# Optimization experiments

Hardware: AMD Instinct MI355X
Metric: run time of the kernel (lower is better)

The kernel has to match this reference:

```python
import jax, jax.numpy as jnp
import numpy as np

VOCAB, SEQ, D_IN, HID, N_CLS, BATCH = 50257, 128, 768, 512, 9, 256


def setup_inputs() -> dict:
    key = jax.random.key(0)
    ks = jax.random.split(key, 12)
    s = 0.02
    return {
        "input_ids": jax.random.randint(ks[0], (BATCH, SEQ), 0, VOCAB),
        "tok_emb": jax.random.normal(ks[1], (VOCAB, D_IN), jnp.float32) * s,
        "pos_emb": jax.random.normal(ks[2], (SEQ, D_IN), jnp.float32) * s,
        # stacked per-gate Linear weights, gate order (i, f, g, o); Linear stores (out, in)
        "W1": jax.random.normal(ks[3], (4, HID, D_IN), jnp.float32) * s,
        "R1": jax.random.normal(ks[4], (4, HID, HID), jnp.float32) * s,
        "b1": jax.random.normal(ks[5], (4, HID), jnp.float32) * s,
        "W2": jax.random.normal(ks[6], (4, HID, HID), jnp.float32) * s,
        "R2": jax.random.normal(ks[7], (4, HID, HID), jnp.float32) * s,
        "b2": jax.random.normal(ks[8], (4, HID), jnp.float32) * s,
        "Wo": jax.random.normal(ks[9], (N_CLS, HID), jnp.float32) * s,
        "bo": jax.random.normal(ks[10], (N_CLS,), jnp.float32) * s,
    }


def _cell(x, h, c, W, R, b):
    # all four gate linears fused into one einsum each for x and h
    g = jnp.einsum('bi,ghi->gbh', x, W) + jnp.einsum('bj,ghj->gbh', h, R) + b[:, None, :]
    i = jax.nn.sigmoid(g[0])
    f = jax.nn.sigmoid(g[1])
    m = jnp.tanh(g[2])
    o = jax.nn.sigmoid(g[3])
    c_next = m * i + f * c
    h_next = o * jnp.tanh(c_next)
    return h_next, c_next


def reference(input_ids, tok_emb, pos_emb, W1, R1, b1, W2, R2, b2, Wo, bo):
    embeds = tok_emb[input_ids] + pos_emb[None, :, :]  # (B, S, D)
    B = embeds.shape[0]
    H = R1.shape[-1]
    x_seq = jnp.swapaxes(embeds, 0, 1)  # (S, B, D)
    init = tuple(jnp.zeros((B, H), embeds.dtype) for _ in range(4))

    def step(carry, x_t):
        h1, c1, h2, c2 = carry
        h1, c1 = _cell(x_t, h1, c1, W1, R1, b1)
        h2, c2 = _cell(h1, h2, c2, W2, R2, b2)
        out = h2 @ Wo.T + bo  # (B, num_class)
        return (h1, c1, h2, c2), out

    _, outs = jax.lax.scan(step, init, x_seq)  # (S, B, C)
    return jnp.swapaxes(outs, 0, 1)  # (B, S, C)
```

## Files before the change

### kernel.cpp

```cpp
#include <hip/hip_runtime.h>
#include <hip/hip_bf16.h>
#include <stdint.h>

#define BATCH_ 256
#define SEQ_   128
#define DIN_   768
#define HID_   512
#define NG_    2048
#define NCLS_  9

typedef unsigned short u16;
typedef unsigned int u32;
typedef unsigned long long u64;
typedef __attribute__((ext_vector_type(8))) short bf16x8;
typedef __attribute__((ext_vector_type(4))) float f32x4;

__device__ __forceinline__ float bf2f(u16 u) {
  return __builtin_bit_cast(float, (uint32_t)u << 16);
}
__device__ __forceinline__ u16 f2bf(float f) {
  uint32_t x = __builtin_bit_cast(uint32_t, f);
  uint32_t r = (x + 0x7fffu + ((x >> 16) & 1u)) >> 16;
  return (u16)r;
}

__device__ __forceinline__ void gload_lds16(const void* g, void* l) {
#if defined(__has_builtin)
#if __has_builtin(__builtin_amdgcn_global_load_lds)
  __builtin_amdgcn_global_load_lds((const __attribute__((address_space(1))) void*)g,
                                   (__attribute__((address_space(3))) void*)l, 16, 0, 0);
  return;
#endif
#endif
  *(uint4*)l = *(const uint4*)g;
}

__device__ __forceinline__ u32 aload32(const u32* p) {
  return __hip_atomic_load(p, __ATOMIC_RELAXED, __HIP_MEMORY_SCOPE_AGENT);
}
__device__ __forceinline__ void astore32(u32* p, u32 v) {
  __hip_atomic_store(p, v, __ATOMIC_RELAXED, __HIP_MEMORY_SCOPE_AGENT);
}

__global__ void castk(const float* __restrict__ s, u16* __restrict__ d, int n4) {
  int i = blockIdx.x * blockDim.x + threadIdx.x;
  if (i < n4) {
    float4 v = ((const float4*)s)[i];
    ushort4 o;
    o.x = f2bf(v.x); o.y = f2bf(v.y); o.z = f2bf(v.z); o.w = f2bf(v.w);
    ((ushort4*)d)[i] = o;
  }
}

__global__ __launch_bounds__(192) void embed_k(const int* __restrict__ ids,
                                               const float* __restrict__ tok,
                                               const float* __restrict__ pos,
                                               u16* __restrict__ X) {
  const int row = blockIdx.x;
  const int t = row >> 8, b = row & 255;
  const int id = ids[b * SEQ_ + t];
  const float4* tr = (const float4*)(tok + (size_t)id * DIN_);
  const float4* pr = (const float4*)(pos + (size_t)t * DIN_);
  const int i = threadIdx.x;
  float4 v = tr[i], p = pr[i];
  ushort4 o;
  o.x = f2bf(v.x + p.x); o.y = f2bf(v.y + p.y);
  o.z = f2bf(v.z + p.z); o.w = f2bf(v.w + p.w);
  ((ushort4*)(X + (size_t)row * DIN_))[i] = o;
}

__global__ __launch_bounds__(256) void gemm_bt(const u16* __restrict__ A,
                                               const u16* __restrict__ Bm,
                                               const float* __restrict__ bias,
                                               u16* __restrict__ C,
                                               int M, int N, int K) {
  __shared__ __align__(16) u16 As[128 * 64];
  __shared__ __align__(16) u16 Bs[128 * 64];
  const int tid = threadIdx.x;
  const int lane = tid & 63;
  const int wave = tid >> 6;
  const int m0 = blockIdx.y * 128;
  const int n0 = blockIdx.x * 128;
  const int wm = (wave >> 1) * 64;
  const int wn = (wave & 1) * 64;
  const int lr = lane & 15;
  const int lg = lane >> 4;
  f32x4 acc[4][4] = {};

  for (int k0 = 0; k0 < K; k0 += 64) {
#pragma unroll
    for (int it = 0; it < 4; ++it) {
      int e = it * 256 + tid;
      int r = e >> 3, c8 = (e & 7) * 8;
      gload_lds16(A + (size_t)(m0 + r) * K + k0 + c8, &As[e * 8]);
      gload_lds16(Bm + (size_t)(n0 + r) * K + k0 + c8, &Bs[e * 8]);
    }
    __syncthreads();
#pragma unroll
    for (int kk = 0; kk < 64; kk += 32) {
      bf16x8 af[4], bfr[4];
#pragma unroll
      for (int i = 0; i < 4; ++i) {
        af[i]  = *(const bf16x8*)&As[(wm + i * 16 + lr) * 64 + kk + lg * 8];
        bfr[i] = *(const bf16x8*)&Bs[(wn + i * 16 + lr) * 64 + kk + lg * 8];
      }
#pragma unroll
      for (int i = 0; i < 4; ++i)
#pragma unroll
        for (int j = 0; j < 4; ++j)
          acc[i][j] = __builtin_amdgcn_mfma_f32_16x16x32_bf16(af[i], bfr[j], acc[i][j], 0, 0, 0);
    }
    __syncthreads();
  }
#pragma unroll
  for (int i = 0; i < 4; ++i) {
#pragma unroll
    for (int j = 0; j < 4; ++j) {
      int col = n0 + wn + j * 16 + lr;
      float bv = bias[col];
#pragma unroll
      for (int q = 0; q < 4; ++q) {
        int row = m0 + wm + i * 16 + lg * 4 + q;
        C[(size_t)row * N + col] = f2bf(acc[i][j][q] + bv);
      }
    }
  }
}

__device__ __forceinline__ void stage64(char* dst, const u16* src, int tid) {
  const u64* s64 = (const u64*)src;
#pragma unroll
  for (int i = 0; i < 16; ++i) {
    int e = i * 512 + tid, r = e >> 7, c8 = e & 127;
    u64 v = s64[(size_t)r * 128 + c8];
    *(u64*)(dst + r * 1024 + ((((c8 >> 1) ^ (r & 7)) << 4) | ((c8 & 1) << 3))) = v;
  }
}

__global__ __launch_bounds__(512, 2) void lstm_duo2(
    const u16* __restrict__ Xpre,
    u16* __restrict__ H1,
    u16* __restrict__ H2,
    const u16* __restrict__ R1b,
    const u16* __restrict__ W2b,
    const u16* __restrict__ R2b,
    const float* __restrict__ b2,
    u32* __restrict__ flag1, u32* __restrict__ flag2) {
  __shared__ __align__(16) char lds[131072];
  const int tid = threadIdx.x;
  const int lane = tid & 63;
  const int w = tid >> 6;
  const int lr = lane & 15, lg = lane >> 4;
  const int kind = blockIdx.x >> 7;
  const int lb = blockIdx.x & 127;
  const int m4 = lb & 3, j32 = lb >> 2;
  const int m0 = m4 * 64, j0 = j32 * 16;
  const int g = w & 3, kh = w >> 2;
  const int cr = tid >> 3, cc = (tid & 7) * 2;
  float* Gsf = (float*)lds;
  char* As1 = lds;
  char* As2 = lds + 65536;

#define GS(KH, GG, RR, CC) Gsf[(((KH) * 4 + (GG)) * 64 + (RR)) * 17 + (CC)]

  if (kind == 0) {
    bf16x8 B1[8];
#pragma unroll
    for (int k = 0; k < 8; ++k)
      B1[k] = *(const bf16x8*)&R1b[(size_t)(g * 512 + j0 + lr) * 512 +
                                   kh * 256 + k * 32 + lg * 8];
    float cst0 = 0.f, cst1 = 0.f;

    for (int t = 0; t < SEQ_; ++t) {
      u32 xp[4];
#pragma unroll
      for (int gg = 0; gg < 4; ++gg)
        xp[gg] = *(const u32*)(Xpre + (size_t)t * (BATCH_ * NG_) +
                               (size_t)(m0 + cr) * NG_ + gg * 512 + j0 + cc);
      if (t > 0) {
        if (w == 0) {
          const u32* f = flag1 + (size_t)(t - 1) * 128 + m4 * 32 + (lane & 31);
          int spins = 0;
          while (!__all(aload32(f) != 0)) {
            __builtin_amdgcn_s_sleep(1);
            if (++spins > (1 << 20)) break;
          }
        }
        __syncthreads();
        stage64(As1, H1 + ((size_t)(t - 1) * BATCH_ + m0) * HID_, tid);
      }
      __syncthreads();
      f32x4 acc[4] = {};
      if (t > 0) {
#pragma unroll
        for (int rf = 0; rf < 4; ++rf) {
#pragma unroll
          for (int k = 0; k < 8; ++k) {
            int c = kh * 32 + k * 4 + lg;
            bf16x8 a = *(const bf16x8*)(As1 + (rf * 16 + lr) * 1024 +
                                        ((c ^ (lr & 7)) << 4));
            acc[rf] = __builtin_amdgcn_mfma_f32_16x16x32_bf16(a, B1[k], acc[rf], 0, 0, 0);
          }
        }
      }
      __syncthreads();
#pragma unroll
      for (int rf = 0; rf < 4; ++rf)
#pragma unroll
        for (int q = 0; q < 4; ++q)
          GS(kh, g, rf * 16 + lg * 4 + q, lr) = acc[rf][q];
      __syncthreads();
      {
        float G[4][2];
#pragma unroll
        for (int gg = 0; gg < 4; ++gg) {
          G[gg][0] = GS(0, gg, cr, cc) + GS(1, gg, cr, cc) + bf2f((u16)xp[gg]);
          G[gg][1] = GS(0, gg, cr, cc + 1) + GS(1, gg, cr, cc + 1) + bf2f((u16)(xp[gg] >> 16));
        }
        u32 pack = 0;
        {
          float iv = 1.f / (1.f + expf(-G[0][0]));
          float fv = 1.f / (1.f + expf(-G[1][0]));
          float mv = tanhf(G[2][0]);
          float ov = 1.f / (1.f + expf(-G[3][0]));
          float cn = mv * iv + fv * cst0; cst0 = cn;
          pack |= (u32)f2bf(ov * tanhf(cn));
        }
        {
          float iv = 1.f / (1.f + expf(-G[0][1]));
          float fv = 1.f / (1.f + expf(-G[1][1]));
          float mv = tanhf(G[2][1]);
          float ov = 1.f / (1.f + expf(-G[3][1]));
          float cn = mv * iv + fv * cst1; cst1 = cn;
          pack |= (u32)f2bf(ov * tanhf(cn)) << 16;
        }
        astore32((u32*)(H1 + (size_t)t * (BATCH_ * HID_) +
                        (size_t)(m0 + cr) * HID_ + j0 + cc), pack);
      }
      __syncthreads();
      if (tid == 0)
        astore32(flag1 + (size_t)t * 128 + m4 * 32 + j32, 1u);
    }
  } else {
    bf16x8 W2f[8], R2f[8];
#pragma unroll
    for (int k = 0; k < 8; ++k) {
      size_t off = (size_t)(g * 512 + j0 + lr) * 512 + kh * 256 + k * 32 + lg * 8;
      W2f[k] = *(const bf16x8*)&W2b[off];
      R2f[k] = *(const bf16x8*)&R2b[off];
    }
    float bc[4][2];
#pragma unroll
    for (int gg = 0; gg < 4; ++gg) {
      bc[gg][0] = b2[gg * 512 + j0 + cc];
      bc[gg][1] = b2[gg * 512 + j0 + cc + 1];
    }
    float cst0 = 0.f, cst1 = 0.f;

    for (int t = 0; t < SEQ_; ++t) {
      if (w == 0) {
        const u32* fa = flag1 + (size_t)t * 128 + m4 * 32 + (lane & 31);
        const u32* fb = flag2 + (size_t)(t > 0 ? t - 1 : 0) * 128 + m4 * 32 + (lane & 31);
        int spins = 0;
        while (true) {
          u32 v = (lane < 32) ? aload32(fa) : ((t > 0) ? aload32(fb) : 1u);
          if (__all(v != 0)) break;
          __builtin_amdgcn_s_sleep(1);
          if (++spins > (1 << 20)) break;
        }
      }
      __syncthreads();
      stage64(As1, H1 + ((size_t)t * BATCH_ + m0) * HID_, tid);
      if (t > 0)
        stage64(As2, H2 + ((size_t)(t - 1) * BATCH_ + m0) * HID_, tid);
      __syncthreads();
      f32x4 acc[4] = {};
#pragma unroll
      for (int rf = 0; rf < 4; ++rf) {
#pragma unroll
        for (int k = 0; k < 8; ++k) {
          int c = kh * 32 + k * 4 + lg;
          bf16x8 a = *(const bf16x8*)(As1 + (rf * 16 + lr) * 1024 +
                                      ((c ^ (lr & 7)) << 4));
          acc[rf] = __builtin_amdgcn_mfma_f32_16x16x32_bf16(a, W2f[k], acc[rf], 0, 0, 0);
        }
      }
      if (t > 0) {
#pragma unroll
        for (int rf = 0; rf < 4; ++rf) {
#pragma unroll
          for (int k = 0; k < 8; ++k) {
            int c = kh * 32 + k * 4 + lg;
            bf16x8 a = *(const bf16x8*)(As2 + (rf * 16 + lr) * 1024 +
                                        ((c ^ (lr & 7)) << 4));
            acc[rf] = __builtin_amdgcn_mfma_f32_16x16x32_bf16(a, R2f[k], acc[rf], 0, 0, 0);
          }
        }
      }
      __syncthreads();
#pragma unroll
      for (int rf = 0; rf < 4; ++rf)
#pragma unroll
        for (int q = 0; q < 4; ++q)
          GS(kh, g, rf * 16 + lg * 4 + q, lr) = acc[rf][q];
      __syncthreads();
      {
        float G[4][2];
#pragma unroll
        for (int gg = 0; gg < 4; ++gg) {
          G[gg][0] = GS(0, gg, cr, cc) + GS(1, gg, cr, cc) + bc[gg][0];
          G[gg][1] = GS(0, gg, cr, cc + 1) + GS(1, gg, cr, cc + 1) + bc[gg][1];
        }
        u32 pack = 0;
        {
          float iv = 1.f / (1.f + expf(-G[0][0]));
          float fv = 1.f / (1.f + expf(-G[1][0]));
          float mv = tanhf(G[2][0]);
          float ov = 1.f / (1.f + expf(-G[3][0]));
          float cn = mv * iv + fv * cst0; cst0 = cn;
          pack |= (u32)f2bf(ov * tanhf(cn));
        }
        {
          float iv = 1.f / (1.f + expf(-G[0][1]));
          float fv = 1.f / (1.f + expf(-G[1][1]));
          float mv = tanhf(G[2][1]);
          float ov = 1.f / (1.f + expf(-G[3][1]));
          float cn = mv * iv + fv * cst1; cst1 = cn;
          pack |= (u32)f2bf(ov * tanhf(cn)) << 16;
        }
        astore32((u32*)(H2 + (size_t)t * (BATCH_ * HID_) +
                        (size_t)(m0 + cr) * HID_ + j0 + cc), pack);
      }
      __syncthreads();
      if (tid == 0)
        astore32(flag2 + (size_t)t * 128 + m4 * 32 + j32, 1u);
    }
  }
#undef GS
}

__global__ __launch_bounds__(320) void out_proj(const u16* __restrict__ H2,
                                                const float* __restrict__ Wo,
                                                const float* __restrict__ bo,
                                                float* __restrict__ out) {
  __shared__ __align__(16) u16 Hs[32 * 520];
  const int r0 = blockIdx.x * 32;
  const int tid = threadIdx.x;
  for (int e = tid; e < 2048; e += 320) {
    int rl = e >> 6, k8 = (e & 63) * 8;
    *(uint4*)&Hs[rl * 520 + k8] = *(const uint4*)(H2 + (size_t)(r0 + rl) * HID_ + k8);
  }
  __syncthreads();
  if (tid < 288) {
    int rl = tid / 9, cls = tid - rl * 9;
    const u16* h = &Hs[rl * 520];
    const float* wv = Wo + cls * HID_;
    float s = bo[cls];
#pragma unroll 8
    for (int k = 0; k < HID_; ++k) s += bf2f(h[k]) * wv[k];
    int r = r0 + rl, t = r >> 8, b = r & 255;
    out[((size_t)b * SEQ_ + t) * NCLS_ + cls] = s;
  }
}

extern "C" void kernel_launch(void* const* d_in, const int* in_sizes, int n_in,
                              void* d_out, int out_size, void* d_ws, size_t ws_size,
                              hipStream_t stream) {
  (void)in_sizes; (void)n_in; (void)out_size; (void)ws_size;
  const int*   ids = (const int*)d_in[0];
  const float* tok = (const float*)d_in[1];
  const float* pos = (const float*)d_in[2];
  const float* W1  = (const float*)d_in[3];
  const float* R1  = (const float*)d_in[4];
  const float* b1  = (const float*)d_in[5];
  const float* W2  = (const float*)d_in[6];
  const float* R2  = (const float*)d_in[7];
  const float* b2  = (const float*)d_in[8];
  const float* Wo  = (const float*)d_in[9];
  const float* bo  = (const float*)d_in[10];
  float* out = (float*)d_out;

  char* p = (char*)d_ws;
  auto alloc = [&](size_t bytes) { char* q = p; p += (bytes + 255) & ~(size_t)255; return q; };
  u16*  W1b  = (u16*)alloc((size_t)NG_ * DIN_ * 2);
  u16*  R1b  = (u16*)alloc((size_t)NG_ * HID_ * 2);
  u16*  W2b  = (u16*)alloc((size_t)NG_ * HID_ * 2);
  u16*  R2b  = (u16*)alloc((size_t)NG_ * HID_ * 2);
  u32*  flag1 = (u32*)alloc((size_t)SEQ_ * 128 * 4);
  u32*  flag2 = (u32*)alloc((size_t)SEQ_ * 128 * 4);
  size_t xbf_bytes = (size_t)SEQ_ * BATCH_ * DIN_ * 2;
  u16*  Xbf  = (u16*)alloc(xbf_bytes);
  u16*  H1all = Xbf;
  u16*  H2all = (u16*)alloc((size_t)SEQ_ * BATCH_ * HID_ * 2);
  u16*  Xpre = (u16*)alloc((size_t)SEQ_ * BATCH_ * NG_ * 2);

  castk<<<dim3((NG_ * DIN_ / 4 + 255) / 256), 256, 0, stream>>>(W1, W1b, NG_ * DIN_ / 4);
  castk<<<dim3((NG_ * HID_ / 4 + 255) / 256), 256, 0, stream>>>(R1, R1b, NG_ * HID_ / 4);
  castk<<<dim3((NG_ * HID_ / 4 + 255) / 256), 256, 0, stream>>>(W2, W2b, NG_ * HID_ / 4);
  castk<<<dim3((NG_ * HID_ / 4 + 255) / 256), 256, 0, stream>>>(R2, R2b, NG_ * HID_ / 4);
  hipMemsetAsync(flag1, 0, (size_t)SEQ_ * 256 * 4, stream);

  embed_k<<<dim3(SEQ_ * BATCH_), 192, 0, stream>>>(ids, tok, pos, Xbf);

  gemm_bt<<<dim3(NG_ / 128, SEQ_ * BATCH_ / 128), 256, 0, stream>>>(
      Xbf, W1b, b1, Xpre, SEQ_ * BATCH_, NG_, DIN_);

  {
    const u16* Xp = Xpre; u16* H1a = H1all; u16* H2a = H2all;
    const u16* R1a = R1b; const u16* W2a = W2b; const u16* R2a = R2b;
    const float* b2a = b2;
    u32* f1 = flag1; u32* f2 = flag2;
    void* args[] = {(void*)&Xp, (void*)&H1a, (void*)&H2a, (void*)&R1a,
                    (void*)&W2a, (void*)&R2a, (void*)&b2a, (void*)&f1, (void*)&f2};
    hipLaunchCooperativeKernel(reinterpret_cast<void*>(&lstm_duo2),
                               dim3(256), dim3(512), args, 0, stream);
  }

  out_proj<<<dim3(SEQ_ * BATCH_ / 32), 320, 0, stream>>>(H2all, Wo, bo, out);
}
```

Measured before the change: 1.110 ms.

## Retile recurrent LSTM blocks to 32x32 and sync via per-row-group counters

Each persistent block now covers 32 batch rows by 32 hidden units per gate instead of 64 by 16. That halves the H staging per block per step and lets each A fragment feed two MFMAs. In layer 2 the two K-halves are split so one warp group multiplies H1 by W2 and the other multiplies H2 by R2, each over the full K. Per-block flag arrays are replaced by atomic counters per row group, waited on by a single lane, so polling traffic drops. The cost is more register pressure from the doubled weight fragments (32 bf16x8 per thread in layer 2) and contention from the atomic adds.

After: 913.1 us. -17.7%, faster.

```diff
diff --git a/kernel.cpp b/kernel.cpp
--- a/kernel.cpp
+++ b/kernel.cpp
@@ -127,17 +127,17 @@
   }
 }
 
-__device__ __forceinline__ void stage64(char* dst, const u16* src, int tid) {
+__device__ __forceinline__ void stage32r(char* dst, const u16* src, int tid) {
   const u64* s64 = (const u64*)src;
 #pragma unroll
-  for (int i = 0; i < 16; ++i) {
+  for (int i = 0; i < 8; ++i) {
     int e = i * 512 + tid, r = e >> 7, c8 = e & 127;
     u64 v = s64[(size_t)r * 128 + c8];
     *(u64*)(dst + r * 1024 + ((((c8 >> 1) ^ (r & 7)) << 4) | ((c8 & 1) << 3))) = v;
   }
 }
 
-__global__ __launch_bounds__(512, 2) void lstm_duo2(
+__global__ __launch_bounds__(512, 2) void lstm_duo3(
     const u16* __restrict__ Xpre,
     u16* __restrict__ H1,
     u16* __restrict__ H2,
@@ -145,30 +145,30 @@
     const u16* __restrict__ W2b,
     const u16* __restrict__ R2b,
     const float* __restrict__ b2,
-    u32* __restrict__ flag1, u32* __restrict__ flag2) {
-  __shared__ __align__(16) char lds[131072];
+    u32* __restrict__ cnt1, u32* __restrict__ cnt2) {
+  __shared__ __align__(16) char As1[32 * 1024];
+  __shared__ __align__(16) char As2[32 * 1024];
+  __shared__ float Gsf[2 * 4 * 32 * 33];
   const int tid = threadIdx.x;
   const int lane = tid & 63;
   const int w = tid >> 6;
   const int lr = lane & 15, lg = lane >> 4;
   const int kind = blockIdx.x >> 7;
   const int lb = blockIdx.x & 127;
-  const int m4 = lb & 3, j32 = lb >> 2;
-  const int m0 = m4 * 64, j0 = j32 * 16;
+  const int m8 = lb & 7, j16 = lb >> 3;
+  const int m0 = m8 * 32, j0 = j16 * 32;
   const int g = w & 3, kh = w >> 2;
-  const int cr = tid >> 3, cc = (tid & 7) * 2;
-  float* Gsf = (float*)lds;
-  char* As1 = lds;
-  char* As2 = lds + 65536;
-
-#define GS(KH, GG, RR, CC) Gsf[(((KH) * 4 + (GG)) * 64 + (RR)) * 17 + (CC)]
+  const int cr = tid >> 4, cc = (tid & 15) * 2;
+#define GS(KH, GG, RR, CC) Gsf[(((KH) * 4 + (GG)) * 32 + (RR)) * 33 + (CC)]
 
   if (kind == 0) {
-    bf16x8 B1[8];
-#pragma unroll
-    for (int k = 0; k < 8; ++k)
-      B1[k] = *(const bf16x8*)&R1b[(size_t)(g * 512 + j0 + lr) * 512 +
-                                   kh * 256 + k * 32 + lg * 8];
+    bf16x8 B1[2][8];
+#pragma unroll
+    for (int nf = 0; nf < 2; ++nf)
+#pragma unroll
+      for (int k = 0; k < 8; ++k)
+        B1[nf][k] = *(const bf16x8*)&R1b[(size_t)(g * 512 + j0 + nf * 16 + lr) * 512 +
+                                         kh * 256 + k * 32 + lg * 8];
     float cst0 = 0.f, cst1 = 0.f;
 
     for (int t = 0; t < SEQ_; ++t) {
@@ -178,37 +178,39 @@
         xp[gg] = *(const u32*)(Xpre + (size_t)t * (BATCH_ * NG_) +
                                (size_t)(m0 + cr) * NG_ + gg * 512 + j0 + cc);
       if (t > 0) {
-        if (w == 0) {
-          const u32* f = flag1 + (size_t)(t - 1) * 128 + m4 * 32 + (lane & 31);
+        if (w == 0 && lane == 0) {
+          const u32* f = cnt1 + (size_t)(t - 1) * 8 + m8;
           int spins = 0;
-          while (!__all(aload32(f) != 0)) {
+          while (aload32(f) < 16u) {
             __builtin_amdgcn_s_sleep(1);
-            if (++spins > (1 << 20)) break;
+            if (++spins > (1 << 21)) break;
           }
         }
         __syncthreads();
-        stage64(As1, H1 + ((size_t)(t - 1) * BATCH_ + m0) * HID_, tid);
-      }
-      __syncthreads();
-      f32x4 acc[4] = {};
+        stage32r(As1, H1 + ((size_t)(t - 1) * BATCH_ + m0) * HID_, tid);
+      }
+      __syncthreads();
+      f32x4 acc[2][2] = {};
       if (t > 0) {
 #pragma unroll
-        for (int rf = 0; rf < 4; ++rf) {
-#pragma unroll
-          for (int k = 0; k < 8; ++k) {
-            int c = kh * 32 + k * 4 + lg;
-            bf16x8 a = *(const bf16x8*)(As1 + (rf * 16 + lr) * 1024 +
-                                        ((c ^ (lr & 7)) << 4));
-            acc[rf] = __builtin_amdgcn_mfma_f32_16x16x32_bf16(a, B1[k], acc[rf], 0, 0, 0);
-          }
-        }
-      }
-      __syncthreads();
-#pragma unroll
-      for (int rf = 0; rf < 4; ++rf)
-#pragma unroll
-        for (int q = 0; q < 4; ++q)
-          GS(kh, g, rf * 16 + lg * 4 + q, lr) = acc[rf][q];
+        for (int k = 0; k < 8; ++k) {
+          int c = kh * 32 + k * 4 + lg;
+          int sw = ((c ^ (lr & 7)) << 4);
+          bf16x8 a0 = *(const bf16x8*)(As1 + (lr) * 1024 + sw);
+          bf16x8 a1 = *(const bf16x8*)(As1 + (16 + lr) * 1024 + sw);
+          acc[0][0] = __builtin_amdgcn_mfma_f32_16x16x32_bf16(a0, B1[0][k], acc[0][0], 0, 0, 0);
+          acc[0][1] = __builtin_amdgcn_mfma_f32_16x16x32_bf16(a0, B1[1][k], acc[0][1], 0, 0, 0);
+          acc[1][0] = __builtin_amdgcn_mfma_f32_16x16x32_bf16(a1, B1[0][k], acc[1][0], 0, 0, 0);
+          acc[1][1] = __builtin_amdgcn_mfma_f32_16x16x32_bf16(a1, B1[1][k], acc[1][1], 0, 0, 0);
+        }
+      }
+#pragma unroll
+      for (int mf = 0; mf < 2; ++mf)
+#pragma unroll
+        for (int nf = 0; nf < 2; ++nf)
+#pragma unroll
+          for (int q = 0; q < 4; ++q)
+            GS(kh, g, mf * 16 + lg * 4 + q, nf * 16 + lr) = acc[mf][nf][q];
       __syncthreads();
       {
         float G[4][2];
@@ -239,16 +241,18 @@
       }
       __syncthreads();
       if (tid == 0)
-        astore32(flag1 + (size_t)t * 128 + m4 * 32 + j32, 1u);
+        __hip_atomic_fetch_add(cnt1 + (size_t)t * 8 + m8, 1u,
+                               __ATOMIC_RELAXED, __HIP_MEMORY_SCOPE_AGENT);
     }
   } else {
-    bf16x8 W2f[8], R2f[8];
-#pragma unroll
-    for (int k = 0; k < 8; ++k) {
-      size_t off = (size_t)(g * 512 + j0 + lr) * 512 + kh * 256 + k * 32 + lg * 8;
-      W2f[k] = *(const bf16x8*)&W2b[off];
-      R2f[k] = *(const bf16x8*)&R2b[off];
-    }
+    const u16* Bmat = kh ? R2b : W2b;
+    bf16x8 Bw[2][16];
+#pragma unroll
+    for (int nf = 0; nf < 2; ++nf)
+#pragma unroll
+      for (int k = 0; k < 16; ++k)
+        Bw[nf][k] = *(const bf16x8*)&Bmat[(size_t)(g * 512 + j0 + nf * 16 + lr) * 512 +
+                                          k * 32 + lg * 8];
     float bc[4][2];
 #pragma unroll
     for (int gg = 0; gg < 4; ++gg) {
@@ -259,50 +263,45 @@
 
     for (int t = 0; t < SEQ_; ++t) {
       if (w == 0) {
-        const u32* fa = flag1 + (size_t)t * 128 + m4 * 32 + (lane & 31);
-        const u32* fb = flag2 + (size_t)(t > 0 ? t - 1 : 0) * 128 + m4 * 32 + (lane & 31);
+        const u32* fa = cnt1 + (size_t)t * 8 + m8;
+        const u32* fb = cnt2 + (size_t)(t > 0 ? t - 1 : 0) * 8 + m8;
         int spins = 0;
         while (true) {
-          u32 v = (lane < 32) ? aload32(fa) : ((t > 0) ? aload32(fb) : 1u);
-          if (__all(v != 0)) break;
+          bool ok = true;
+          if (lane == 0) ok = aload32(fa) >= 16u;
+          else if (lane == 1) ok = (t == 0) || (aload32(fb) >= 16u);
+          if (__all(ok)) break;
           __builtin_amdgcn_s_sleep(1);
-          if (++spins > (1 << 20)) break;
-        }
-      }
-      __syncthreads();
-      stage64(As1, H1 + ((size_t)t * BATCH_ + m0) * HID_, tid);
+          if (++spins > (1 << 21)) break;
+        }
+      }
+      __syncthreads();
+      stage32r(As1, H1 + ((size_t)t * BATCH_ + m0) * HID_, tid);
       if (t > 0)
-        stage64(As2, H2 + ((size_t)(t - 1) * BATCH_ + m0) * HID_, tid);
-      __syncthreads();
-      f32x4 acc[4] = {};
-#pragma unroll
-      for (int rf = 0; rf < 4; ++rf) {
-#pragma unroll
-        for (int k = 0; k < 8; ++k) {
-          int c = kh * 32 + k * 4 + lg;
-          bf16x8 a = *(const bf16x8*)(As1 + (rf * 16 + lr) * 1024 +
-                                      ((c ^ (lr & 7)) << 4));
-          acc[rf] = __builtin_amdgcn_mfma_f32_16x16x32_bf16(a, W2f[k], acc[rf], 0, 0, 0);
-        }
-      }
-      if (t > 0) {
-#pragma unroll
-        for (int rf = 0; rf < 4; ++rf) {
-#pragma unroll
-          for (int k = 0; k < 8; ++k) {
-            int c = kh * 32 + k * 4 + lg;
-            bf16x8 a = *(const bf16x8*)(As2 + (rf * 16 + lr) * 1024 +
-                                        ((c ^ (lr & 7)) << 4));
-            acc[rf] = __builtin_amdgcn_mfma_f32_16x16x32_bf16(a, R2f[k], acc[rf], 0, 0, 0);
-          }
-        }
-      }
-      __syncthreads();
-#pragma unroll
-      for (int rf = 0; rf < 4; ++rf)
-#pragma unroll
-        for (int q = 0; q < 4; ++q)
-          GS(kh, g, rf * 16 + lg * 4 + q, lr) = acc[rf][q];
+        stage32r(As2, H2 + ((size_t)(t - 1) * BATCH_ + m0) * HID_, tid);
+      __syncthreads();
+      f32x4 acc[2][2] = {};
+      if (kh == 0 || t > 0) {
+        const char* As = kh ? As2 : As1;
+#pragma unroll
+        for (int k = 0; k < 16; ++k) {
+          int c = k * 4 + lg;
+          int sw = ((c ^ (lr & 7)) << 4);
+          bf16x8 a0 = *(const bf16x8*)(As + (lr) * 1024 + sw);
+          bf16x8 a1 = *(const bf16x8*)(As + (16 + lr) * 1024 + sw);
+          acc[0][0] = __builtin_amdgcn_mfma_f32_16x16x32_bf16(a0, Bw[0][k], acc[0][0], 0, 0, 0);
+          acc[0][1] = __builtin_amdgcn_mfma_f32_16x16x32_bf16(a0, Bw[1][k], acc[0][1], 0, 0, 0);
+          acc[1][0] = __builtin_amdgcn_mfma_f32_16x16x32_bf16(a1, Bw[0][k], acc[1][0], 0, 0, 0);
+          acc[1][1] = __builtin_amdgcn_mfma_f32_16x16x32_bf16(a1, Bw[1][k], acc[1][1], 0, 0, 0);
+        }
+      }
+#pragma unroll
+      for (int mf = 0; mf < 2; ++mf)
+#pragma unroll
+        for (int nf = 0; nf < 2; ++nf)
+#pragma unroll
+          for (int q = 0; q < 4; ++q)
+            GS(kh, g, mf * 16 + lg * 4 + q, nf * 16 + lr) = acc[mf][nf][q];
       __syncthreads();
       {
         float G[4][2];
@@ -333,7 +332,8 @@
       }
       __syncthreads();
       if (tid == 0)
-        astore32(flag2 + (size_t)t * 128 + m4 * 32 + j32, 1u);
+        __hip_atomic_fetch_add(cnt2 + (size_t)t * 8 + m8, 1u,
+                               __ATOMIC_RELAXED, __HIP_MEMORY_SCOPE_AGENT);
     }
   }
 #undef GS
@@ -386,8 +386,8 @@
   u16*  R1b  = (u16*)alloc((size_t)NG_ * HID_ * 2);
   u16*  W2b  = (u16*)alloc((size_t)NG_ * HID_ * 2);
   u16*  R2b  = (u16*)alloc((size_t)NG_ * HID_ * 2);
-  u32*  flag1 = (u32*)alloc((size_t)SEQ_ * 128 * 4);
-  u32*  flag2 = (u32*)alloc((size_t)SEQ_ * 128 * 4);
+  u32*  cnt1 = (u32*)alloc((size_t)SEQ_ * 8 * 4);
+  u32*  cnt2 = (u32*)alloc((size_t)SEQ_ * 8 * 4);
   size_t xbf_bytes = (size_t)SEQ_ * BATCH_ * DIN_ * 2;
   u16*  Xbf  = (u16*)alloc(xbf_bytes);
   u16*  H1all = Xbf;
@@ -398,7 +398,7 @@
   castk<<<dim3((NG_ * HID_ / 4 + 255) / 256), 256, 0, stream>>>(R1, R1b, NG_ * HID_ / 4);
   castk<<<dim3((NG_ * HID_ / 4 + 255) / 256), 256, 0, stream>>>(W2, W2b, NG_ * HID_ / 4);
   castk<<<dim3((NG_ * HID_ / 4 + 255) / 256), 256, 0, stream>>>(R2, R2b, NG_ * HID_ / 4);
-  hipMemsetAsync(flag1, 0, (size_t)SEQ_ * 256 * 4, stream);
+  hipMemsetAsync(cnt1, 0, (size_t)2 * SEQ_ * 8 * 4, stream);
 
   embed_k<<<dim3(SEQ_ * BATCH_), 192, 0, stream>>>(ids, tok, pos, Xbf);
 
@@ -409,10 +409,10 @@
     const u16* Xp = Xpre; u16* H1a = H1all; u16* H2a = H2all;
     const u16* R1a = R1b; const u16* W2a = W2b; const u16* R2a = R2b;
     const float* b2a = b2;
-    u32* f1 = flag1; u32* f2 = flag2;
+    u32* c1 = cnt1; u32* c2 = cnt2;
     void* args[] = {(void*)&Xp, (void*)&H1a, (void*)&H2a, (void*)&R1a,
-                    (void*)&W2a, (void*)&R2a, (void*)&b2a, (void*)&f1, (void*)&f2};
-    hipLaunchCooperativeKernel(reinterpret_cast<void*>(&lstm_duo2),
+                    (void*)&W2a, (void*)&R2a, (void*)&b2a, (void*)&c1, (void*)&c2};
+    hipLaunchCooperativeKernel(reinterpret_cast<void*>(&lstm_duo3),
                                dim3(256), dim3(512), args, 0, stream);
   }
 
```
